# Kernel optimization log

Measured on AMD Instinct MI355X. Metric: run time of the kernel, lower is better.

The kernel has to match this reference:

```python
import jax, jax.numpy as jnp
import numpy as np

EPS = 1e-8  # torch F.cosine_similarity default eps


def setup_inputs() -> dict:
    key = jax.random.key(0)
    k1, k2 = jax.random.split(key)
    x = jax.random.normal(k1, (16384, 1024), dtype=jnp.float32)
    label = jax.random.randint(k2, (16384, 64), 0, 2).astype(jnp.int64)
    w = jnp.asarray(10.0, dtype=jnp.float32)  # nn.Parameter init_w
    b = jnp.asarray(-5.0, dtype=jnp.float32)  # nn.Parameter init_b
    return {"x": x, "label": label, "w": w, "b": b}


def reference(x, label, w, b):
    # Append the 'no-label' column for rows whose label vector is all zero.
    extra = (label.sum(axis=1) == 0).astype(label.dtype)[:, None]
    lab = jnp.concatenate([label, extra], axis=1).astype(x.dtype)  # [B, C]

    counts = lab.sum(axis=0)                  # [C] positives per centroid
    active = counts > 0                       # torch drops empty columns; we mask them

    # Centroids: mean of x over rows carrying each label (scatter-mean as GEMM).
    anchor = (lab.T @ x) / jnp.maximum(counts, 1.0)[:, None]   # [C, D]

    # Cosine similarity between every sample and every centroid.
    xn = jnp.maximum(jnp.linalg.norm(x, axis=1), EPS)          # [B]
    an = jnp.maximum(jnp.linalg.norm(anchor, axis=1), EPS)     # [C]
    cos = (x @ anchor.T) / (xn[:, None] * an[None, :])          # [B, C]

    logits = cos * w + b
    # Removing empty columns from softmax == setting their logits to -inf.
    logits = jnp.where(active[None, :], logits, -jnp.inf)
    logp = jax.nn.log_softmax(logits, axis=1)                   # [B, C]

    # Row expansion in torch duplicates sample i once per positive label j;
    # the logits row only depends on i, so CE over expanded rows is a
    # pair-weighted mean of -logp[i, j] over positive (i, j) pairs.
    n_pairs = lab.sum()
    nloss = -jnp.sum(jnp.where(lab > 0, logp, 0.0)) / n_pairs
    return nloss
```

## Files before the change

### kernel.cpp

```cpp
#include <hip/hip_runtime.h>
#include <hip/hip_bf16.h>
#include <stdint.h>

#define NROWS 16384
#define NDIM  1024
#define NLAB  64
#define NC    65
#define CPAD  80

typedef float float4v __attribute__((ext_vector_type(4)));
typedef short short8  __attribute__((ext_vector_type(8)));

static constexpr size_t SCALE_B = 0;
static constexpr size_t ACTB_B  = 320;
static constexpr size_t WSUM_B  = 400;
static constexpr size_t CTR_B   = 404;
static constexpr size_t CNTF_B  = 448;
static constexpr size_t CNTP_B  = 1024;
static constexpr size_t MASK_B  = 83968;
static constexpr size_t XN2_B   = 215040;
static constexpr size_t LFRAG_B = 280576;
static constexpr size_t BFRAG_B = 2902016;
static constexpr size_t XAF_B   = 3065856;
static constexpr size_t XCOL_B  = 36620288;
static constexpr size_t PART_B  = 70174720;
static constexpr size_t SLAB    = (size_t)CPAD * NDIM * 4;

__device__ __forceinline__ unsigned short bf16u(float f) {
    __hip_bfloat16 h = __float2bfloat16(f);
    return __builtin_bit_cast(unsigned short, h);
}
__device__ __forceinline__ unsigned pk2(float a, float b) {
    return (unsigned)bf16u(a) | ((unsigned)bf16u(b) << 16);
}

__global__ __launch_bounds__(256) void k01_prep(const float* __restrict__ x,
                                                const int* __restrict__ label,
                                                unsigned short* __restrict__ xAfrag,
                                                unsigned short* __restrict__ xcol,
                                                float* __restrict__ xn2g,
                                                unsigned long long* __restrict__ masks,
                                                unsigned* __restrict__ cntpart,
                                                unsigned short* __restrict__ lfrag) {
    __shared__ unsigned short xt[16][1034];
    __shared__ unsigned cnt[NC];
    __shared__ unsigned long long smask[64];
    int t = threadIdx.x;
    if (blockIdx.x < 1024) {
        int rt = blockIdx.x;
        int r = t >> 4, cpos = t & 15;
        const float* src = x + ((size_t)rt * 16 + r) * NDIM + cpos * 4;
        float sq = 0.f;
#pragma unroll
        for (int i = 0; i < 16; ++i) {
            float4 f = *(const float4*)(src + i * 64);
            sq += f.x * f.x + f.y * f.y + f.z * f.z + f.w * f.w;
            *(uint2*)&xt[r][cpos * 4 + i * 64] = make_uint2(pk2(f.x, f.y), pk2(f.z, f.w));
        }
#pragma unroll
        for (int m = 1; m < 16; m <<= 1) sq += __shfl_xor(sq, m, 16);
        if (cpos == 0) xn2g[rt * 16 + r] = sq;
        __syncthreads();
        {
            int slot = t & 63, wv = t >> 6;
            int q = slot >> 4, col = slot & 15;
#pragma unroll
            for (int s = 0; s < 8; ++s) {
                int kb = s * 4 + wv;
                uint4 v = *(const uint4*)&xt[col][kb * 32 + q * 8];
                ((uint4*)xAfrag)[((size_t)rt * 32 + kb) * 64 + slot] = v;
            }
        }
#pragma unroll
        for (int s = 0; s < 8; ++s) {
            int dim = s * 128 + (t >> 1);
            int rh = (t & 1) * 8;
            unsigned short tmp[8];
#pragma unroll
            for (int j = 0; j < 8; ++j) tmp[j] = xt[rh + j][dim];
            uint4 v;
            v.x = (unsigned)tmp[0] | ((unsigned)tmp[1] << 16);
            v.y = (unsigned)tmp[2] | ((unsigned)tmp[3] << 16);
            v.z = (unsigned)tmp[4] | ((unsigned)tmp[5] << 16);
            v.w = (unsigned)tmp[6] | ((unsigned)tmp[7] << 16);
            ((uint4*)xcol)[(size_t)rt * 2048 + s * 256 + t] = v;
        }
        return;
    }
    int bid = blockIdx.x - 1024;
    if (t < NC) cnt[t] = 0;
    __syncthreads();
    int wave = t >> 6, lane = t & 63;
    int rowblock = bid * 64;
    unsigned creg = 0, zreg = 0;
#pragma unroll 4
    for (int p = 0; p < 16; ++p) {
        int row = rowblock + p * 4 + wave;
        int v = label[row * NLAB + lane];
        unsigned long long m = __ballot(v != 0);
        creg += (unsigned)((m >> lane) & 1ull);
        if (lane == 0) {
            masks[row] = m;
            smask[p * 4 + wave] = m;
            zreg += (m == 0ull) ? 1u : 0u;
        }
    }
    atomicAdd(&cnt[lane], creg);
    if (lane == 0 && zreg) atomicAdd(&cnt[64], zreg);
    __syncthreads();
    if (t < 80) cntpart[bid * 80 + t] = (t < NC) ? cnt[t] : 0u;
    for (int pid = t; pid < 640; pid += 256) {
        int rt2l = pid / 320, rem = pid % 320;
        int ct = rem >> 6, ln = rem & 63;
        int q = ln >> 4, col = ln & 15;
        int c = ct * 16 + col;
        int rbase = rt2l * 32 + q * 8;
        unsigned pk[4];
#pragma unroll
        for (int jp = 0; jp < 4; ++jp) {
            unsigned long long m0 = smask[rbase + jp * 2], m1 = smask[rbase + jp * 2 + 1];
            unsigned b0, b1;
            if (c < 64)       { b0 = (unsigned)((m0 >> c) & 1ull); b1 = (unsigned)((m1 >> c) & 1ull); }
            else if (c == 64) { b0 = (m0 == 0ull); b1 = (m1 == 0ull); }
            else              { b0 = 0u; b1 = 0u; }
            pk[jp] = (b0 ? 0x3F80u : 0u) | (b1 ? 0x3F800000u : 0u);
        }
        uint4 w = make_uint4(pk[0], pk[1], pk[2], pk[3]);
        ((uint4*)lfrag)[((size_t)(bid * 2 + rt2l) * 5 + ct) * 64 + ln] = w;
    }
}

__global__ __launch_bounds__(256, 4) void k2_sums(const unsigned short* __restrict__ xcol,
                                                  const unsigned short* __restrict__ lfrag,
                                                  float* __restrict__ partial,
                                                  int kslices) {
    int t = threadIdx.x, wave = t >> 6, lane = t & 63;
    int q = lane >> 4, col = lane & 15;
    int dgroup = blockIdx.x & 15, ks = blockIdx.x >> 4;
    int nkb = (NROWS / kslices) >> 5;
    int kb0 = ks * nkb;
    int d = dgroup * 64 + wave * 16 + col;
    const uint4* B = (const uint4*)xcol;
    const uint4* A = (const uint4*)lfrag;
    size_t bidx0 = (size_t)d * 2 + (q & 1);
    int qh = q >> 1;

    float4v acc[5];
#pragma unroll
    for (int ct = 0; ct < 5; ++ct) acc[ct] = (float4v){0.f, 0.f, 0.f, 0.f};

#pragma unroll 4
    for (int i = 0; i < nkb; ++i) {
        int kb = kb0 + i;
        uint4 braw = B[(size_t)(kb * 2 + qh) * 2048 + bidx0];
        short8 bf = __builtin_bit_cast(short8, braw);
#pragma unroll
        for (int ct = 0; ct < 5; ++ct) {
            uint4 araw = A[((size_t)kb * 5 + ct) * 64 + lane];
            short8 af = __builtin_bit_cast(short8, araw);
            acc[ct] = __builtin_amdgcn_mfma_f32_16x16x32_bf16(af, bf, acc[ct], 0, 0, 0);
        }
    }
    float* pb = partial + (size_t)ks * CPAD * NDIM;
#pragma unroll
    for (int ct = 0; ct < 5; ++ct)
#pragma unroll
        for (int reg = 0; reg < 4; ++reg)
            pb[(size_t)(ct * 16 + q * 4 + reg) * NDIM + d] = acc[ct][reg];
}

__global__ __launch_bounds__(256) void k2b_fuse(const float* __restrict__ wptr,
                                                const unsigned* __restrict__ cntpart,
                                                const float* __restrict__ partial,
                                                int kslices,
                                                unsigned short* __restrict__ bfrag,
                                                float* __restrict__ scale,
                                                unsigned char* __restrict__ actB,
                                                unsigned* __restrict__ countsF,
                                                float* __restrict__ wsum,
                                                unsigned* __restrict__ counter) {
    int c = blockIdx.x, t = threadIdx.x;
    __shared__ float red[8];
    __shared__ unsigned credu[4];
    if (c == 0 && t == 1) { *wsum = 0.f; *counter = 0u; }
    unsigned cv = cntpart[t * 80 + c];
#pragma unroll
    for (int m = 32; m >= 1; m >>= 1) cv += __shfl_xor(cv, m, 64);
    if ((t & 63) == 0) credu[t >> 6] = cv;
    __syncthreads();
    unsigned cnt = credu[0] + credu[1] + credu[2] + credu[3];

    int d0 = t * 4;
    const float* p = partial + (size_t)c * NDIM + d0;
    float4 s = make_float4(0.f, 0.f, 0.f, 0.f);
#pragma unroll 8
    for (int sl = 0; sl < kslices; ++sl) {
        float4 v = *(const float4*)(p + (size_t)sl * CPAD * NDIM);
        s.x += v.x; s.y += v.y; s.z += v.z; s.w += v.w;
    }
    float invc = 1.0f / (float)(cnt > 0u ? cnt : 1u);
    float ax = s.x * invc, ay = s.y * invc, az = s.z * invc, aw = s.w * invc;
    float ss = ax * ax + ay * ay + az * az + aw * aw;
#pragma unroll
    for (int m = 32; m >= 1; m >>= 1) ss += __shfl_xor(ss, m, 64);
    if ((t & 63) == 0) red[t >> 6] = ss;
    __syncthreads();
    ss = red[0] + red[1] + red[2] + red[3];

    float denom = fmaxf(sqrtf(ss), 1e-8f);
    float rinv = invc / denom;
    unsigned short h0 = bf16u(s.x * rinv), h1 = bf16u(s.y * rinv);
    unsigned short h2 = bf16u(s.z * rinv), h3 = bf16u(s.w * rinv);
    int ct = c >> 4, colc = c & 15;
    int kb = d0 >> 5, q = (d0 >> 3) & 3, j0 = d0 & 7;
    size_t sidx = ((((size_t)ct * 32 + kb) * 64) + q * 16 + colc) * 8 + j0;
    *(uint2*)(bfrag + sidx) =
        make_uint2(((unsigned)h1 << 16) | h0, ((unsigned)h3 << 16) | h2);

    float f0 = __bfloat162float(__builtin_bit_cast(__hip_bfloat16, h0));
    float f1 = __bfloat162float(__builtin_bit_cast(__hip_bfloat16, h1));
    float f2 = __bfloat162float(__builtin_bit_cast(__hip_bfloat16, h2));
    float f3 = __bfloat162float(__builtin_bit_cast(__hip_bfloat16, h3));
    float nb2 = f0 * f0 + f1 * f1 + f2 * f2 + f3 * f3;
#pragma unroll
    for (int m = 32; m >= 1; m >>= 1) nb2 += __shfl_xor(nb2, m, 64);
    if ((t & 63) == 0) red[4 + (t >> 6)] = nb2;
    __syncthreads();
    if (t == 0) {
        float n2 = red[4] + red[5] + red[6] + red[7];
        scale[c] = (n2 > 0.f) ? (wptr[0] / sqrtf(n2)) : 0.f;
        actB[c] = (cnt > 0u) ? 1 : 0;
        countsF[c] = cnt;
    }
}

__global__ __launch_bounds__(256, 4) void k3_loss(const unsigned short* __restrict__ xAfrag,
                                                  const unsigned short* __restrict__ bfrag,
                                                  const float* __restrict__ xn2g,
                                                  const unsigned long long* __restrict__ masks,
                                                  const unsigned char* __restrict__ actB,
                                                  const float* __restrict__ scale,
                                                  const unsigned* __restrict__ countsF,
                                                  const float* __restrict__ bptr,
                                                  float* __restrict__ wsum,
                                                  unsigned* __restrict__ counter,
                                                  float* __restrict__ out) {
    __shared__ float xch[3][64 * 20];
    int t = threadIdx.x, kh = t >> 6, lane = t & 63;
    int q = lane >> 4, col = lane & 15;
    int rt = blockIdx.x;
    int rowbase = rt * 16;
    const uint4* A = (const uint4*)xAfrag;
    const uint4* B = (const uint4*)bfrag;

    float4v acc[5];
#pragma unroll
    for (int ct = 0; ct < 5; ++ct) acc[ct] = (float4v){0.f, 0.f, 0.f, 0.f};

#pragma unroll
    for (int s = 0; s < 8; ++s) {
        int kb = kh * 8 + s;
        uint4 araw = A[((size_t)rt * 32 + kb) * 64 + lane];
        short8 af = __builtin_bit_cast(short8, araw);
#pragma unroll
        for (int ct = 0; ct < 5; ++ct) {
            uint4 braw = B[((size_t)ct * 32 + kb) * 64 + lane];
            short8 bf = __builtin_bit_cast(short8, braw);
            acc[ct] = __builtin_amdgcn_mfma_f32_16x16x32_bf16(af, bf, acc[ct], 0, 0, 0);
        }
    }
    if (kh) {
        float* dst = &xch[kh - 1][lane * 20];
#pragma unroll
        for (int ct = 0; ct < 5; ++ct)
#pragma unroll
            for (int r = 0; r < 4; ++r) dst[ct * 4 + r] = acc[ct][r];
    }
    __syncthreads();
    if (kh) return;
#pragma unroll
    for (int j = 0; j < 3; ++j) {
        const float* src = &xch[j][lane * 20];
#pragma unroll
        for (int ct = 0; ct < 5; ++ct)
#pragma unroll
            for (int r = 0; r < 4; ++r) acc[ct][r] += src[ct * 4 + r];
    }

    float bv = bptr[0];
    float sc[5]; unsigned char ab[5];
#pragma unroll
    for (int ct = 0; ct < 5; ++ct) { sc[ct] = scale[ct * 16 + col]; ab[ct] = actB[ct * 16 + col]; }

    float contrib = 0.f;
#pragma unroll
    for (int reg = 0; reg < 4; ++reg) {
        int rl = q * 4 + reg;
        int row = rowbase + rl;
        float inv = 1.0f / fmaxf(sqrtf(xn2g[row]), 1e-8f);
        unsigned long long mask = masks[row];
        float v[5]; float lmax = -1e30f;
#pragma unroll
        for (int ct = 0; ct < 5; ++ct) {
            float lg = acc[ct][reg] * sc[ct] * inv + bv;
            v[ct] = ab[ct] ? lg : -1e30f;
            lmax = fmaxf(lmax, v[ct]);
        }
#pragma unroll
        for (int m = 1; m < 16; m <<= 1) lmax = fmaxf(lmax, __shfl_xor(lmax, m, 16));
        float es = 0.f;
#pragma unroll
        for (int ct = 0; ct < 5; ++ct) es += expf(v[ct] - lmax);
#pragma unroll
        for (int m = 1; m < 16; m <<= 1) es += __shfl_xor(es, m, 16);
        float lse = lmax + logf(es);
        float ps = 0.f;
#pragma unroll
        for (int ct = 0; ct < 5; ++ct) {
            int c = ct * 16 + col;
            bool pos = (c < 64) ? (((mask >> c) & 1ull) != 0ull)
                                : ((c == 64) ? (mask == 0ull) : false);
            ps += pos ? v[ct] : 0.f;
        }
#pragma unroll
        for (int m = 1; m < 16; m <<= 1) ps += __shfl_xor(ps, m, 16);
        float npos = mask ? (float)__popcll(mask) : 1.0f;
        float crow = ps - npos * lse;
        if (col == 0) contrib += crow;
    }
#pragma unroll
    for (int m = 1; m < 64; m <<= 1) contrib += __shfl_xor(contrib, m, 64);
    if (lane == 0) {
        atomicAdd(wsum, contrib);
        __threadfence();
        unsigned old = atomicAdd(counter, 1u);
        if (old == (unsigned)gridDim.x - 1u) {
            float np = 0.f;
            for (int c = 0; c < NC; ++c) np += (float)countsF[c];
            float tot = atomicAdd(wsum, 0.0f);
            out[0] = -tot / np;
        }
    }
}

extern "C" void kernel_launch(void* const* d_in, const int* in_sizes, int n_in,
                              void* d_out, int out_size, void* d_ws, size_t ws_size,
                              hipStream_t stream) {
    (void)in_sizes; (void)n_in; (void)out_size;
    const float* x = (const float*)d_in[0];
    const int* label = (const int*)d_in[1];
    const float* w = (const float*)d_in[2];
    const float* b = (const float*)d_in[3];

    char* ws = (char*)d_ws;
    float* scale = (float*)(ws + SCALE_B);
    unsigned char* actB = (unsigned char*)(ws + ACTB_B);
    float* wsum = (float*)(ws + WSUM_B);
    unsigned* counter = (unsigned*)(ws + CTR_B);
    unsigned* countsF = (unsigned*)(ws + CNTF_B);
    unsigned* cntpart = (unsigned*)(ws + CNTP_B);
    unsigned long long* masks = (unsigned long long*)(ws + MASK_B);
    float* xn2g = (float*)(ws + XN2_B);
    unsigned short* lfrag = (unsigned short*)(ws + LFRAG_B);
    unsigned short* bfrag = (unsigned short*)(ws + BFRAG_B);
    unsigned short* xAfrag = (unsigned short*)(ws + XAF_B);
    unsigned short* xcol = (unsigned short*)(ws + XCOL_B);
    float* partial = (float*)(ws + PART_B);

    int kslices = 64;
    while (kslices > 8 && PART_B + (size_t)kslices * SLAB > ws_size) kslices >>= 1;

    hipLaunchKernelGGL(k01_prep, dim3(1024 + 256), dim3(256), 0, stream,
                       x, label, xAfrag, xcol, xn2g, masks, cntpart, lfrag);
    hipLaunchKernelGGL(k2_sums, dim3(16 * kslices), dim3(256), 0, stream,
                       xcol, lfrag, partial, kslices);
    hipLaunchKernelGGL(k2b_fuse, dim3(CPAD), dim3(256), 0, stream,
                       w, cntpart, partial, kslices, bfrag, scale, actB, countsF, wsum, counter);
    hipLaunchKernelGGL(k3_loss, dim3(NROWS / 16), dim3(256), 0, stream,
                       xAfrag, bfrag, xn2g, masks, actB, scale, countsF, b, wsum, counter,
                       (float*)d_out);
}
```

Before: 178.5 us.

## Software-pipeline GEMM loads, restructure loss kernel per-wave, add final reduction kernel

The k2_sums and k3_loss main loops become double-buffered, so the loads for the next k-blocks are issued before the MFMAs that consume the current ones. k3_loss changes from splitting K across four waves and reducing through shared memory to giving each wave its own 16-row tile with the full K loop, which removes the LDS exchange and the barrier. k2b_fuse now runs 1024 threads per centroid, one per dimension, kslices drops from 64 to 32, and the atomic last-block counter is replaced by a separate one-thread finalize kernel. These trade an extra launch and fewer split-K blocks for less synchronization and better latency hiding.

```diff
diff --git a/kernel.cpp b/kernel.cpp
--- a/kernel.cpp
+++ b/kernel.cpp
@@ -14,7 +14,6 @@
 static constexpr size_t SCALE_B = 0;
 static constexpr size_t ACTB_B  = 320;
 static constexpr size_t WSUM_B  = 400;
-static constexpr size_t CTR_B   = 404;
 static constexpr size_t CNTF_B  = 448;
 static constexpr size_t CNTP_B  = 1024;
 static constexpr size_t MASK_B  = 83968;
@@ -130,10 +129,10 @@
     }
 }
 
-__global__ __launch_bounds__(256, 4) void k2_sums(const unsigned short* __restrict__ xcol,
-                                                  const unsigned short* __restrict__ lfrag,
-                                                  float* __restrict__ partial,
-                                                  int kslices) {
+__global__ __launch_bounds__(256) void k2_sums(const unsigned short* __restrict__ xcol,
+                                               const unsigned short* __restrict__ lfrag,
+                                               float* __restrict__ partial,
+                                               int kslices) {
     int t = threadIdx.x, wave = t >> 6, lane = t & 63;
     int q = lane >> 4, col = lane & 15;
     int dgroup = blockIdx.x & 15, ks = blockIdx.x >> 4;
@@ -149,16 +148,39 @@
 #pragma unroll
     for (int ct = 0; ct < 5; ++ct) acc[ct] = (float4v){0.f, 0.f, 0.f, 0.f};
 
-#pragma unroll 4
-    for (int i = 0; i < nkb; ++i) {
-        int kb = kb0 + i;
-        uint4 braw = B[(size_t)(kb * 2 + qh) * 2048 + bidx0];
-        short8 bf = __builtin_bit_cast(short8, braw);
-#pragma unroll
-        for (int ct = 0; ct < 5; ++ct) {
-            uint4 araw = A[((size_t)kb * 5 + ct) * 64 + lane];
-            short8 af = __builtin_bit_cast(short8, araw);
-            acc[ct] = __builtin_amdgcn_mfma_f32_16x16x32_bf16(af, bf, acc[ct], 0, 0, 0);
+    uint4 b0 = B[(size_t)((kb0 + 0) * 2 + qh) * 2048 + bidx0];
+    uint4 a0[5];
+#pragma unroll
+    for (int ct = 0; ct < 5; ++ct) a0[ct] = A[((size_t)(kb0 + 0) * 5 + ct) * 64 + lane];
+    uint4 b1 = B[(size_t)((kb0 + 1) * 2 + qh) * 2048 + bidx0];
+    uint4 a1[5];
+#pragma unroll
+    for (int ct = 0; ct < 5; ++ct) a1[ct] = A[((size_t)(kb0 + 1) * 5 + ct) * 64 + lane];
+
+    for (int i = 0; i < nkb; i += 2) {
+        int p2 = i + 2 < nkb ? kb0 + i + 2 : kb0 + i;
+        int p3 = i + 3 < nkb ? kb0 + i + 3 : kb0 + i + 1;
+        {
+            short8 bf = __builtin_bit_cast(short8, b0);
+#pragma unroll
+            for (int ct = 0; ct < 5; ++ct) {
+                short8 af = __builtin_bit_cast(short8, a0[ct]);
+                acc[ct] = __builtin_amdgcn_mfma_f32_16x16x32_bf16(af, bf, acc[ct], 0, 0, 0);
+            }
+            b0 = B[(size_t)(p2 * 2 + qh) * 2048 + bidx0];
+#pragma unroll
+            for (int ct = 0; ct < 5; ++ct) a0[ct] = A[((size_t)p2 * 5 + ct) * 64 + lane];
+        }
+        {
+            short8 bf = __builtin_bit_cast(short8, b1);
+#pragma unroll
+            for (int ct = 0; ct < 5; ++ct) {
+                short8 af = __builtin_bit_cast(short8, a1[ct]);
+                acc[ct] = __builtin_amdgcn_mfma_f32_16x16x32_bf16(af, bf, acc[ct], 0, 0, 0);
+            }
+            b1 = B[(size_t)(p3 * 2 + qh) * 2048 + bidx0];
+#pragma unroll
+            for (int ct = 0; ct < 5; ++ct) a1[ct] = A[((size_t)p3 * 5 + ct) * 64 + lane];
         }
     }
     float* pb = partial + (size_t)ks * CPAD * NDIM;
@@ -169,122 +191,120 @@
             pb[(size_t)(ct * 16 + q * 4 + reg) * NDIM + d] = acc[ct][reg];
 }
 
-__global__ __launch_bounds__(256) void k2b_fuse(const float* __restrict__ wptr,
-                                                const unsigned* __restrict__ cntpart,
-                                                const float* __restrict__ partial,
-                                                int kslices,
-                                                unsigned short* __restrict__ bfrag,
-                                                float* __restrict__ scale,
-                                                unsigned char* __restrict__ actB,
-                                                unsigned* __restrict__ countsF,
-                                                float* __restrict__ wsum,
-                                                unsigned* __restrict__ counter) {
+__global__ __launch_bounds__(1024) void k2b_fuse(const float* __restrict__ wptr,
+                                                 const unsigned* __restrict__ cntpart,
+                                                 const float* __restrict__ partial,
+                                                 int kslices,
+                                                 unsigned short* __restrict__ bfrag,
+                                                 float* __restrict__ scale,
+                                                 unsigned char* __restrict__ actB,
+                                                 unsigned* __restrict__ countsF,
+                                                 float* __restrict__ wsum) {
     int c = blockIdx.x, t = threadIdx.x;
-    __shared__ float red[8];
+    __shared__ float red[16];
     __shared__ unsigned credu[4];
-    if (c == 0 && t == 1) { *wsum = 0.f; *counter = 0u; }
-    unsigned cv = cntpart[t * 80 + c];
-#pragma unroll
-    for (int m = 32; m >= 1; m >>= 1) cv += __shfl_xor(cv, m, 64);
-    if ((t & 63) == 0) credu[t >> 6] = cv;
+    __shared__ float bcast[2];
+    if (c == 0 && t == 512) *wsum = 0.f;
+    if (t < 256) {
+        unsigned cv = cntpart[t * 80 + c];
+#pragma unroll
+        for (int m = 32; m >= 1; m >>= 1) cv += __shfl_xor(cv, m, 64);
+        if ((t & 63) == 0) credu[t >> 6] = cv;
+    }
     __syncthreads();
     unsigned cnt = credu[0] + credu[1] + credu[2] + credu[3];
 
-    int d0 = t * 4;
-    const float* p = partial + (size_t)c * NDIM + d0;
-    float4 s = make_float4(0.f, 0.f, 0.f, 0.f);
+    const float* p = partial + (size_t)c * NDIM + t;
+    float s = 0.f;
 #pragma unroll 8
-    for (int sl = 0; sl < kslices; ++sl) {
-        float4 v = *(const float4*)(p + (size_t)sl * CPAD * NDIM);
-        s.x += v.x; s.y += v.y; s.z += v.z; s.w += v.w;
-    }
+    for (int sl = 0; sl < kslices; ++sl)
+        s += p[(size_t)sl * CPAD * NDIM];
     float invc = 1.0f / (float)(cnt > 0u ? cnt : 1u);
-    float ax = s.x * invc, ay = s.y * invc, az = s.z * invc, aw = s.w * invc;
-    float ss = ax * ax + ay * ay + az * az + aw * aw;
+    float a = s * invc;
+    float ss = a * a;
 #pragma unroll
     for (int m = 32; m >= 1; m >>= 1) ss += __shfl_xor(ss, m, 64);
     if ((t & 63) == 0) red[t >> 6] = ss;
     __syncthreads();
-    ss = red[0] + red[1] + red[2] + red[3];
-
-    float denom = fmaxf(sqrtf(ss), 1e-8f);
-    float rinv = invc / denom;
-    unsigned short h0 = bf16u(s.x * rinv), h1 = bf16u(s.y * rinv);
-    unsigned short h2 = bf16u(s.z * rinv), h3 = bf16u(s.w * rinv);
+    if (t == 0) {
+        float tot = 0.f;
+#pragma unroll
+        for (int j = 0; j < 16; ++j) tot += red[j];
+        bcast[0] = fmaxf(sqrtf(tot), 1e-8f);
+    }
+    __syncthreads();
+    float rinv = 1.0f / bcast[0];
+    unsigned short h = bf16u(a * rinv);
     int ct = c >> 4, colc = c & 15;
-    int kb = d0 >> 5, q = (d0 >> 3) & 3, j0 = d0 & 7;
-    size_t sidx = ((((size_t)ct * 32 + kb) * 64) + q * 16 + colc) * 8 + j0;
-    *(uint2*)(bfrag + sidx) =
-        make_uint2(((unsigned)h1 << 16) | h0, ((unsigned)h3 << 16) | h2);
-
-    float f0 = __bfloat162float(__builtin_bit_cast(__hip_bfloat16, h0));
-    float f1 = __bfloat162float(__builtin_bit_cast(__hip_bfloat16, h1));
-    float f2 = __bfloat162float(__builtin_bit_cast(__hip_bfloat16, h2));
-    float f3 = __bfloat162float(__builtin_bit_cast(__hip_bfloat16, h3));
-    float nb2 = f0 * f0 + f1 * f1 + f2 * f2 + f3 * f3;
+    int kb = t >> 5, q = (t >> 3) & 3, j0 = t & 7;
+    bfrag[((((size_t)ct * 32 + kb) * 64) + q * 16 + colc) * 8 + j0] = h;
+    float hv = __bfloat162float(__builtin_bit_cast(__hip_bfloat16, h));
+    float nb2 = hv * hv;
 #pragma unroll
     for (int m = 32; m >= 1; m >>= 1) nb2 += __shfl_xor(nb2, m, 64);
-    if ((t & 63) == 0) red[4 + (t >> 6)] = nb2;
+    if ((t & 63) == 0) red[t >> 6] = nb2;
     __syncthreads();
     if (t == 0) {
-        float n2 = red[4] + red[5] + red[6] + red[7];
+        float n2 = 0.f;
+#pragma unroll
+        for (int j = 0; j < 16; ++j) n2 += red[j];
         scale[c] = (n2 > 0.f) ? (wptr[0] / sqrtf(n2)) : 0.f;
         actB[c] = (cnt > 0u) ? 1 : 0;
         countsF[c] = cnt;
     }
 }
 
-__global__ __launch_bounds__(256, 4) void k3_loss(const unsigned short* __restrict__ xAfrag,
-                                                  const unsigned short* __restrict__ bfrag,
-                                                  const float* __restrict__ xn2g,
-                                                  const unsigned long long* __restrict__ masks,
-                                                  const unsigned char* __restrict__ actB,
-                                                  const float* __restrict__ scale,
-                                                  const unsigned* __restrict__ countsF,
-                                                  const float* __restrict__ bptr,
-                                                  float* __restrict__ wsum,
-                                                  unsigned* __restrict__ counter,
-                                                  float* __restrict__ out) {
-    __shared__ float xch[3][64 * 20];
-    int t = threadIdx.x, kh = t >> 6, lane = t & 63;
+__global__ __launch_bounds__(256) void k3_loss(const unsigned short* __restrict__ xAfrag,
+                                               const unsigned short* __restrict__ bfrag,
+                                               const float* __restrict__ xn2g,
+                                               const unsigned long long* __restrict__ masks,
+                                               const unsigned char* __restrict__ actB,
+                                               const float* __restrict__ scale,
+                                               const float* __restrict__ bptr,
+                                               float* __restrict__ wsum) {
+    int t = threadIdx.x, wave = t >> 6, lane = t & 63;
     int q = lane >> 4, col = lane & 15;
-    int rt = blockIdx.x;
+    int rt = blockIdx.x * 4 + wave;
     int rowbase = rt * 16;
-    const uint4* A = (const uint4*)xAfrag;
-    const uint4* B = (const uint4*)bfrag;
+    const uint4* A = (const uint4*)xAfrag + (size_t)rt * 32 * 64 + lane;
+    const uint4* Bp = (const uint4*)bfrag + lane;
 
     float4v acc[5];
 #pragma unroll
     for (int ct = 0; ct < 5; ++ct) acc[ct] = (float4v){0.f, 0.f, 0.f, 0.f};
 
-#pragma unroll
-    for (int s = 0; s < 8; ++s) {
-        int kb = kh * 8 + s;
-        uint4 araw = A[((size_t)rt * 32 + kb) * 64 + lane];
-        short8 af = __builtin_bit_cast(short8, araw);
-#pragma unroll
-        for (int ct = 0; ct < 5; ++ct) {
-            uint4 braw = B[((size_t)ct * 32 + kb) * 64 + lane];
-            short8 bf = __builtin_bit_cast(short8, braw);
-            acc[ct] = __builtin_amdgcn_mfma_f32_16x16x32_bf16(af, bf, acc[ct], 0, 0, 0);
-        }
-    }
-    if (kh) {
-        float* dst = &xch[kh - 1][lane * 20];
-#pragma unroll
-        for (int ct = 0; ct < 5; ++ct)
-#pragma unroll
-            for (int r = 0; r < 4; ++r) dst[ct * 4 + r] = acc[ct][r];
-    }
-    __syncthreads();
-    if (kh) return;
-#pragma unroll
-    for (int j = 0; j < 3; ++j) {
-        const float* src = &xch[j][lane * 20];
-#pragma unroll
-        for (int ct = 0; ct < 5; ++ct)
-#pragma unroll
-            for (int r = 0; r < 4; ++r) acc[ct][r] += src[ct * 4 + r];
+    uint4 a0 = A[0], a1 = A[64];
+    uint4 b0[5], b1[5];
+#pragma unroll
+    for (int ct = 0; ct < 5; ++ct) b0[ct] = Bp[(size_t)(ct * 32 + 0) * 64];
+#pragma unroll
+    for (int ct = 0; ct < 5; ++ct) b1[ct] = Bp[(size_t)(ct * 32 + 1) * 64];
+
+    for (int s = 0; s < 32; s += 2) {
+        int p2 = s + 2 < 32 ? s + 2 : s;
+        int p3 = s + 3 < 32 ? s + 3 : s + 1;
+        {
+            short8 af = __builtin_bit_cast(short8, a0);
+#pragma unroll
+            for (int ct = 0; ct < 5; ++ct) {
+                short8 bf = __builtin_bit_cast(short8, b0[ct]);
+                acc[ct] = __builtin_amdgcn_mfma_f32_16x16x32_bf16(af, bf, acc[ct], 0, 0, 0);
+            }
+            a0 = A[p2 * 64];
+#pragma unroll
+            for (int ct = 0; ct < 5; ++ct) b0[ct] = Bp[(size_t)(ct * 32 + p2) * 64];
+        }
+        {
+            short8 af = __builtin_bit_cast(short8, a1);
+#pragma unroll
+            for (int ct = 0; ct < 5; ++ct) {
+                short8 bf = __builtin_bit_cast(short8, b1[ct]);
+                acc[ct] = __builtin_amdgcn_mfma_f32_16x16x32_bf16(af, bf, acc[ct], 0, 0, 0);
+            }
+            a1 = A[p3 * 64];
+#pragma unroll
+            for (int ct = 0; ct < 5; ++ct) b1[ct] = Bp[(size_t)(ct * 32 + p3) * 64];
+        }
     }
 
     float bv = bptr[0];
@@ -330,16 +350,16 @@
     }
 #pragma unroll
     for (int m = 1; m < 64; m <<= 1) contrib += __shfl_xor(contrib, m, 64);
-    if (lane == 0) {
-        atomicAdd(wsum, contrib);
-        __threadfence();
-        unsigned old = atomicAdd(counter, 1u);
-        if (old == (unsigned)gridDim.x - 1u) {
-            float np = 0.f;
-            for (int c = 0; c < NC; ++c) np += (float)countsF[c];
-            float tot = atomicAdd(wsum, 0.0f);
-            out[0] = -tot / np;
-        }
+    if (lane == 0) atomicAdd(wsum, contrib);
+}
+
+__global__ void k4_final(const unsigned* __restrict__ countsF,
+                         const float* __restrict__ wsum,
+                         float* __restrict__ out) {
+    if (threadIdx.x == 0 && blockIdx.x == 0) {
+        float np = 0.f;
+        for (int c = 0; c < NC; ++c) np += (float)countsF[c];
+        out[0] = -wsum[0] / np;
     }
 }
 
@@ -356,7 +376,6 @@
     float* scale = (float*)(ws + SCALE_B);
     unsigned char* actB = (unsigned char*)(ws + ACTB_B);
     float* wsum = (float*)(ws + WSUM_B);
-    unsigned* counter = (unsigned*)(ws + CTR_B);
     unsigned* countsF = (unsigned*)(ws + CNTF_B);
     unsigned* cntpart = (unsigned*)(ws + CNTP_B);
     unsigned long long* masks = (unsigned long long*)(ws + MASK_B);
@@ -367,16 +386,16 @@
     unsigned short* xcol = (unsigned short*)(ws + XCOL_B);
     float* partial = (float*)(ws + PART_B);
 
-    int kslices = 64;
+    int kslices = 32;
     while (kslices > 8 && PART_B + (size_t)kslices * SLAB > ws_size) kslices >>= 1;
 
     hipLaunchKernelGGL(k01_prep, dim3(1024 + 256), dim3(256), 0, stream,
                        x, label, xAfrag, xcol, xn2g, masks, cntpart, lfrag);
     hipLaunchKernelGGL(k2_sums, dim3(16 * kslices), dim3(256), 0, stream,
                        xcol, lfrag, partial, kslices);
-    hipLaunchKernelGGL(k2b_fuse, dim3(CPAD), dim3(256), 0, stream,
-                       w, cntpart, partial, kslices, bfrag, scale, actB, countsF, wsum, counter);
-    hipLaunchKernelGGL(k3_loss, dim3(NROWS / 16), dim3(256), 0, stream,
-                       xAfrag, bfrag, xn2g, masks, actB, scale, countsF, b, wsum, counter,
-                       (float*)d_out);
-}
+    hipLaunchKernelGGL(k2b_fuse, dim3(CPAD), dim3(1024), 0, stream,
+                       w, cntpart, partial, kslices, bfrag, scale, actB, countsF, wsum);
+    hipLaunchKernelGGL(k3_loss, dim3(NROWS / 64), dim3(256), 0, stream,
+                       xAfrag, bfrag, xn2g, masks, actB, scale, b, wsum);
+    hipLaunchKernelGGL(k4_final, dim3(1), dim3(64), 0, stream, countsF, wsum, (float*)d_out);
+}
```

Measured after the change: 161.6 us. 1.1x faster.
